# Kernel tuning notes

Measured on AMD Instinct MI355X. Metric: run time of the kernel, lower is better.

The kernel has to match this reference:

```python
import jax, jax.numpy as jnp
import numpy as np

B, G, S, L, F = 2, 1024, 64, 16, 8   # batch, attention windows, tokens/window, cells/token, in_features
ATT, RANK, HC = 128, 32, 32          # att_dim, factorization rank, n_head_channels
LF = L * F


def setup_inputs() -> dict:
    key = jax.random.key(0)
    ks = jax.random.split(key, 14)
    s = 0.05
    return {
        "x": jax.random.normal(ks[0], (B, G, S, L, F), jnp.float32),
        # rank-factorized Q projection: (L*F) -> att_dim
        "Wq_u": jax.random.normal(ks[1], (LF, RANK), jnp.float32) * s,
        "Wq_v": jax.random.normal(ks[2], (RANK, ATT), jnp.float32) * s,
        # rank-factorized KV projection: (L*F) -> 2*att_dim (bias=True in source)
        "Wkv_u": jax.random.normal(ks[3], (LF, RANK), jnp.float32) * s,
        "Wkv_v": jax.random.normal(ks[4], (RANK, 2 * ATT), jnp.float32) * s,
        "kv_b": jnp.zeros((2 * ATT,), jnp.float32),
        # rank-factorized out layer: att_dim -> (L*F)
        "Wo_u": jax.random.normal(ks[5], (ATT, RANK), jnp.float32) * s,
        "Wo_v": jax.random.normal(ks[6], (RANK, LF), jnp.float32) * s,
        # per-token-element residual gate (init 1e-7 as in source)
        "gamma": jnp.full((L, F), 1e-7, jnp.float32),
        # factorized MLP: (L*F) -> att_dim -> (L*F)
        "W1": jax.random.normal(ks[7], (LF, ATT), jnp.float32) * s,
        "b1": jnp.zeros((ATT,), jnp.float32),
        "W2": jax.random.normal(ks[8], (ATT, LF), jnp.float32) * s,
        "b2": jnp.zeros((LF,), jnp.float32),
        "gamma_mlp": jnp.full((), 1e-7, jnp.float32),
    }


def _ln(t):
    # layer norm over the token dims (L, F), no affine
    m = t.mean(axis=(-2, -1), keepdims=True)
    v = t.var(axis=(-2, -1), keepdims=True)
    return (t - m) * jax.lax.rsqrt(v + 1e-5)


def reference(x, Wq_u, Wq_v, Wkv_u, Wkv_v, kv_b, Wo_u, Wo_v, gamma, W1, b1, W2, b2, gamma_mlp):
    b, g, sfx, l, f = x.shape
    lf = l * f
    h = _ln(x).reshape(b, g, sfx, lf)                 # [b,g,s,LF]
    q = (h @ Wq_u) @ Wq_v                              # [b,g,s,ATT]
    kv = (h @ Wkv_u) @ Wkv_v + kv_b                    # [b,g,s,2*ATT]
    k, v = jnp.split(kv, 2, axis=-1)
    nh = q.shape[-1] // HC
    def heads(t):
        return t.reshape(b, g, sfx, nh, HC).transpose(0, 1, 3, 2, 4)  # [b,g,H,s,hc]
    qh, kh, vh = heads(q), heads(k), heads(v)
    scores = jnp.einsum('bghsc,bghtc->bghst', qh, kh) / np.float32(np.sqrt(HC))
    attn = jax.nn.softmax(scores, axis=-1)             # [b,g,H,s,s]
    o = jnp.einsum('bghst,bghtc->bghsc', attn, vh)
    o = o.transpose(0, 1, 3, 2, 4).reshape(b, g, sfx, nh * HC)
    upd = ((o @ Wo_u) @ Wo_v).reshape(b, g, sfx, l, f)
    x1 = x + gamma * upd                               # 'shift' update with gamma gate
    h2 = _ln(x1).reshape(b, g, sfx, lf)
    m = jax.nn.gelu(h2 @ W1 + b1) @ W2 + b2
    return x1 + gamma_mlp * m.reshape(b, g, sfx, l, f)
```

## Files before the change

### kernel.cpp

```cpp
#include <hip/hip_runtime.h>

#define NWIN 2048

#define WUT8_OFF 0
#define MT8_OFF  8192
#define OT8_OFF  12288
#define W1T_OFF  28672
#define W2T8_OFF 61440
#define CVEC_OFF 77824

typedef __attribute__((ext_vector_type(8))) __bf16 bf16x8;
typedef __attribute__((ext_vector_type(8))) short s16x8;
typedef __attribute__((ext_vector_type(4))) short s16x4;
typedef __attribute__((ext_vector_type(4))) float f32x4;

static __device__ inline short f2bf(float f) {
    __bf16 b = (__bf16)f;
    return __builtin_bit_cast(short, b);
}
static __device__ inline float bf2f(short h) {
    unsigned u = ((unsigned)(unsigned short)h) << 16;
    return __builtin_bit_cast(float, u);
}
static __device__ inline bf16x8 ldbf8(const short* p) {
    return __builtin_bit_cast(bf16x8, *(const s16x8*)p);
}
static __device__ inline unsigned char f2fp8(float v) {
    return (unsigned char)__builtin_amdgcn_cvt_pk_fp8_f32(v, v, 0u, false);
}
static __device__ inline long ld8(const void* p) {
    return *(const long*)p;
}

__global__ __launch_bounds__(256) void fam_pre(
    const float* __restrict__ Wq_u, const float* __restrict__ Wq_v,
    const float* __restrict__ Wkv_u, const float* __restrict__ Wkv_v,
    const float* __restrict__ kv_b, const float* __restrict__ Wo_u,
    const float* __restrict__ Wo_v, const float* __restrict__ W1,
    const float* __restrict__ W2, unsigned char* __restrict__ ws8)
{
    const int b = blockIdx.x, tid = threadIdx.x;
    float* cvec = (float*)(ws8 + CVEC_OFF);
    if (b < 16) {
        __shared__ float Wv[4096];
        __shared__ float Wu[4096];
        __shared__ float N[4096];
        for (int i = tid; i < 4096; i += 256) {
            int r = i >> 7, c = i & 127;
            Wv[i] = Wkv_v[r*256 + 128 + c];
            Wu[i] = Wo_u[i];
        }
        __syncthreads();
        for (int i = tid; i < 4096; i += 256) {
            int h = i >> 10, u = (i >> 5) & 31, r = i & 31;
            float acc = 0.f;
            for (int c = 0; c < 32; ++c) acc += Wv[r*128 + h*32 + c] * Wu[(h*32 + c)*32 + u];
            N[i] = acc;
        }
        __syncthreads();
        for (int i = tid; i < 1024; i += 256) {
            int jj = i >> 7, hr = i & 127;
            int j = b*8 + jj, h = hr >> 5, r = hr & 31;
            float acc = 0.f;
            for (int u = 0; u < 32; ++u) acc += N[h*1024 + u*32 + r] * Wo_v[u*128 + j];
            ws8[OT8_OFF + j*128 + hr] = f2fp8(acc * 128.f);
        }
    } else if (b < 32) {
        short* w1t = (short*)(ws8 + W1T_OFF);
        int i0 = (b - 16) * 8;
        for (int t = tid; t < 1024; t += 256) {
            int ii = t >> 7, k = t & 127, i = i0 + ii;
            w1t[i*128 + k] = f2bf(W1[k*128 + i]);
        }
    } else if (b < 48) {
        int j0 = (b - 32) * 8;
        for (int t = tid; t < 1024; t += 256) {
            int jj = t >> 7, k = t & 127, j = j0 + jj;
            ws8[W2T8_OFF + j*128 + k] = f2fp8(W2[k*128 + j] * 16.f);
        }
    } else {
        __shared__ float Aq[4096];
        __shared__ float Ak[4096];
        __shared__ float ov[32];
        for (int i = tid; i < 4096; i += 256) {
            int r = i >> 7, c = i & 127;
            Aq[i] = Wq_v[i];
            Ak[i] = Wkv_v[r*256 + c];
        }
        for (int i = tid; i < 8192; i += 256) {
            int n = i >> 7, k = i & 127;
            float w = (n < 32) ? Wq_u[k*32 + n] : Wkv_u[k*32 + (n - 32)];
            ws8[WUT8_OFF + n*128 + k] = f2fp8(w * 16.f);
        }
        __syncthreads();
        const float sc = 0.17677669529663687f * 256.f;
        for (int i = tid; i < 4096; i += 256) {
            int h = i >> 10, r = (i >> 5) & 31, u = i & 31;
            float acc = 0.f;
            for (int c = 0; c < 32; ++c) acc += Aq[u*128 + h*32 + c] * Ak[r*128 + h*32 + c];
            ws8[MT8_OFF + h*1024 + r*32 + u] = f2fp8(acc * sc);
        }
        if (tid < 32) {
            float a = 0.f;
            for (int att = 0; att < 128; ++att) a += kv_b[128 + att] * Wo_u[att*32 + tid];
            ov[tid] = a;
        }
        __syncthreads();
        if (tid < 128) {
            float a = 0.f;
            for (int u = 0; u < 32; ++u) a += ov[u] * Wo_v[u*128 + tid];
            cvec[tid] = a;
        }
    }
}

#define SRA 136
#define SHQ 40
#define SHB 72

#define SM_RA8   0
#define SM_HUQ8  8704
#define SM_KV8   11264
#define SM_KVT8  13824
#define SM_HB8   16128
#define SM_TOTAL 34560

__global__ __launch_bounds__(256, 4) void fam_main(
    const float* __restrict__ x, const unsigned char* __restrict__ ws8,
    const float* __restrict__ gamma, const float* __restrict__ b1,
    const float* __restrict__ b2, const float* __restrict__ gmlp_p,
    float* __restrict__ out)
{
    __shared__ __align__(16) unsigned char SM[SM_TOTAL];
    unsigned char* RA8  = SM + SM_RA8;
    unsigned char* HUQ8 = SM + SM_HUQ8;
    unsigned char* KV8  = SM + SM_KV8;
    unsigned char* KVT8 = SM + SM_KVT8;

    const float* cvec = (const float*)(ws8 + CVEC_OFF);
    const int tid = threadIdx.x;
    const int l   = tid & 63;
    const int wv  = tid >> 6;
    const int l15 = l & 15;
    const int lg  = l >> 4;
    const size_t base = (size_t)blockIdx.x * 8192;
    const float* __restrict__ xw   = x + base;
    float* __restrict__       outw = out + base;
    const int n0 = wv * 32;

    {
        int s = tid >> 2, c = tid & 3;
        float4 xr1[8];
        float sum = 0.f, sq = 0.f;
        #pragma unroll
        for (int j = 0; j < 8; ++j) {
            xr1[j] = *(const float4*)&xw[s*128 + c*32 + j*4];
            sum += xr1[j].x + xr1[j].y + xr1[j].z + xr1[j].w;
            sq  += xr1[j].x*xr1[j].x + xr1[j].y*xr1[j].y + xr1[j].z*xr1[j].z + xr1[j].w*xr1[j].w;
        }
        sum += __shfl_xor(sum, 1); sq += __shfl_xor(sq, 1);
        sum += __shfl_xor(sum, 2); sq += __shfl_xor(sq, 2);
        float mean = sum * (1.f/128.f);
        float var  = sq * (1.f/128.f) - mean*mean;
        float rinv = rsqrtf(var + 1e-5f);
        #pragma unroll
        for (int j = 0; j < 8; ++j) {
            unsigned w = 0;
            w = __builtin_amdgcn_cvt_pk_fp8_f32((xr1[j].x - mean)*rinv, (xr1[j].y - mean)*rinv, w, false);
            w = __builtin_amdgcn_cvt_pk_fp8_f32((xr1[j].z - mean)*rinv, (xr1[j].w - mean)*rinv, w, true);
            *(unsigned*)&RA8[s*SRA + c*32 + j*4] = w;
        }
    }
    __syncthreads();

    {
        long bfr[4];
        #pragma unroll
        for (int kb = 0; kb < 4; ++kb)
            bfr[kb] = ld8(ws8 + WUT8_OFF + (wv*16 + l15)*128 + kb*32 + lg*8);
        #pragma unroll
        for (int m = 0; m < 4; ++m) {
            f32x4 acc = {0.f, 0.f, 0.f, 0.f};
            #pragma unroll
            for (int kb = 0; kb < 4; ++kb) {
                long a = ld8(RA8 + (m*16 + l15)*SRA + kb*32 + lg*8);
                acc = __builtin_amdgcn_mfma_f32_16x16x32_fp8_fp8(a, bfr[kb], acc, 0, 0, 0);
            }
            if (wv < 2) {
                int col = wv*16 + l15;
                #pragma unroll
                for (int j = 0; j < 4; ++j)
                    HUQ8[(m*16 + lg*4 + j)*SHQ + col] = f2fp8(acc[j] * 0.25f);
            } else {
                int u = (wv - 2)*16 + l15;
                #pragma unroll
                for (int j = 0; j < 4; ++j)
                    KV8[(m*16 + lg*4 + j)*SHQ + u] = f2fp8(acc[j] * 0.25f);
                unsigned w = 0;
                w = __builtin_amdgcn_cvt_pk_fp8_f32(acc[0]*0.25f, acc[1]*0.25f, w, false);
                w = __builtin_amdgcn_cvt_pk_fp8_f32(acc[2]*0.25f, acc[3]*0.25f, w, true);
                *(unsigned*)&KVT8[u*SHB + m*16 + lg*4] = w;
            }
        }
    }
    __syncthreads();

    {
        const int h = wv;
        unsigned char* HB8h = SM + SM_HB8 + h*4608;
        long bm0 = ld8(ws8 + MT8_OFF + h*1024 + l15*32 + lg*8);
        long bm1 = ld8(ws8 + MT8_OFF + h*1024 + (16 + l15)*32 + lg*8);
        #pragma unroll
        for (int m = 0; m < 4; ++m) {
            long aq = ld8(HUQ8 + (m*16 + l15)*SHQ + lg*8);
            f32x4 z = {0.f, 0.f, 0.f, 0.f};
            f32x4 a0 = __builtin_amdgcn_mfma_f32_16x16x32_fp8_fp8(aq, bm0, z, 0, 0, 0);
            f32x4 a1 = __builtin_amdgcn_mfma_f32_16x16x32_fp8_fp8(aq, bm1, z, 0, 0, 0);
            #pragma unroll
            for (int j = 0; j < 4; ++j) {
                int row = (m*16 + lg*4 + j)*SHB;
                HB8h[row + l15]      = f2fp8(a0[j] * 0.0625f);
                HB8h[row + 16 + l15] = f2fp8(a1[j] * 0.0625f);
            }
        }
        long av[4], bq[4];
        #pragma unroll
        for (int m = 0; m < 4; ++m) av[m] = ld8(KV8 + (m*16 + l15)*SHQ + lg*8);
        #pragma unroll
        for (int n = 0; n < 4; ++n) bq[n] = ld8(HB8h + (n*16 + l15)*SHB + lg*8);
        f32x4 cc[4][4];
        #pragma unroll
        for (int m = 0; m < 4; ++m)
            #pragma unroll
            for (int n = 0; n < 4; ++n) {
                f32x4 z = {0.f, 0.f, 0.f, 0.f};
                cc[m][n] = __builtin_amdgcn_mfma_f32_16x16x32_fp8_fp8(av[m], bq[n], z, 0, 0, 0);
            }
        const float c1 = 0.0056355275f;
        #pragma unroll
        for (int n = 0; n < 4; ++n) {
            float e[4][4];
            float sm = 0.f;
            #pragma unroll
            for (int m = 0; m < 4; ++m)
                #pragma unroll
                for (int j = 0; j < 4; ++j) {
                    e[m][j] = exp2f(fminf(cc[m][n][j] * c1, 43.f));
                    sm += e[m][j];
                }
            sm += __shfl_xor(sm, 16);
            sm += __shfl_xor(sm, 32);
            float rs64 = __builtin_amdgcn_rcpf(sm) * 64.f;
            int srow = (n*16 + l15) * SHB;
            #pragma unroll
            for (int m = 0; m < 4; ++m) {
                unsigned w = 0;
                w = __builtin_amdgcn_cvt_pk_fp8_f32(e[m][0]*rs64, e[m][1]*rs64, w, false);
                w = __builtin_amdgcn_cvt_pk_fp8_f32(e[m][2]*rs64, e[m][3]*rs64, w, true);
                *(unsigned*)&HB8h[srow + m*16 + lg*4] = w;
            }
        }
        long a8[4][2], b8[2][2];
        #pragma unroll
        for (int m = 0; m < 4; ++m)
            #pragma unroll
            for (int kb = 0; kb < 2; ++kb)
                a8[m][kb] = ld8(HB8h + (m*16 + l15)*SHB + kb*32 + lg*8);
        #pragma unroll
        for (int nn = 0; nn < 2; ++nn)
            #pragma unroll
            for (int kb = 0; kb < 2; ++kb)
                b8[nn][kb] = ld8(KVT8 + (nn*16 + l15)*SHB + kb*32 + lg*8);
        #pragma unroll
        for (int m = 0; m < 4; ++m)
            #pragma unroll
            for (int nn = 0; nn < 2; ++nn) {
                f32x4 acc = {0.f,0.f,0.f,0.f};
                acc = __builtin_amdgcn_mfma_f32_16x16x32_fp8_fp8(a8[m][0], b8[nn][0], acc, 0, 0, 0);
                acc = __builtin_amdgcn_mfma_f32_16x16x32_fp8_fp8(a8[m][1], b8[nn][1], acc, 0, 0, 0);
                #pragma unroll
                for (int j = 0; j < 4; ++j)
                    RA8[(m*16 + lg*4 + j)*SRA + h*32 + nn*16 + l15] = f2fp8(acc[j] * 0.03125f);
            }
    }
    __syncthreads();

    float x1v[4][2][4];
    short* XB = (short*)(SM + SM_HB8);

    {
        float xr[4][2][4];
        #pragma unroll
        for (int m = 0; m < 4; ++m)
            #pragma unroll
            for (int nn = 0; nn < 2; ++nn)
                #pragma unroll
                for (int j = 0; j < 4; ++j)
                    xr[m][nn][j] = xw[(m*16 + lg*4 + j)*128 + n0 + nn*16 + l15];
        long bo[2][4];
        float cv[2], gm[2];
        #pragma unroll
        for (int nn = 0; nn < 2; ++nn) {
            int col = n0 + nn*16 + l15;
            #pragma unroll
            for (int kb = 0; kb < 4; ++kb)
                bo[nn][kb] = ld8(ws8 + OT8_OFF + col*128 + kb*32 + lg*8);
            cv[nn] = cvec[col];
            gm[nn] = gamma[col];
        }
        f32x4 acc[4][2];
        #pragma unroll
        for (int m = 0; m < 4; ++m)
            #pragma unroll
            for (int nn = 0; nn < 2; ++nn) acc[m][nn] = (f32x4){0.f,0.f,0.f,0.f};
        #pragma unroll
        for (int m = 0; m < 4; ++m) {
            long a[4];
            #pragma unroll
            for (int kb = 0; kb < 4; ++kb)
                a[kb] = ld8(RA8 + (m*16 + l15)*SRA + kb*32 + lg*8);
            #pragma unroll
            for (int kb = 0; kb < 4; ++kb)
                #pragma unroll
                for (int nn = 0; nn < 2; ++nn)
                    acc[m][nn] = __builtin_amdgcn_mfma_f32_16x16x32_fp8_fp8(a[kb], bo[nn][kb], acc[m][nn], 0, 0, 0);
        }
        #pragma unroll
        for (int m = 0; m < 4; ++m)
            #pragma unroll
            for (int nn = 0; nn < 2; ++nn)
                #pragma unroll
                for (int j = 0; j < 4; ++j) {
                    int row = m*16 + lg*4 + j;
                    float v = xr[m][nn][j] + gm[nn] * (acc[m][nn][j] * 9.765625e-4f + cv[nn]);
                    x1v[m][nn][j] = v;
                    XB[row*SRA + n0 + nn*16 + l15] = f2bf(v);
                }
    }
    __syncthreads();

    {
        int s = tid >> 2, c = tid & 3;
        float sum = 0.f, sq = 0.f;
        #pragma unroll
        for (int jj = 0; jj < 8; ++jj) {
            s16x4 hv = *(const s16x4*)&XB[s*SRA + c*32 + jj*4];
            #pragma unroll
            for (int e = 0; e < 4; ++e) {
                float f = bf2f(hv[e]);
                sum += f; sq += f*f;
            }
        }
        sum += __shfl_xor(sum, 1); sq += __shfl_xor(sq, 1);
        sum += __shfl_xor(sum, 2); sq += __shfl_xor(sq, 2);
        float mean = sum * (1.f/128.f);
        float var  = sq * (1.f/128.f) - mean*mean;
        float rinv = rsqrtf(var + 1e-5f);
        #pragma unroll
        for (int jj = 0; jj < 8; ++jj) {
            s16x4 hv = *(const s16x4*)&XB[s*SRA + c*32 + jj*4];
            s16x4 ov;
            #pragma unroll
            for (int e = 0; e < 4; ++e) ov[e] = f2bf((bf2f(hv[e]) - mean) * rinv);
            *(s16x4*)&XB[s*SRA + c*32 + jj*4] = ov;
        }
    }
    __syncthreads();

    {
        const short* W1t = (const short*)(ws8 + W1T_OFF);
        bf16x8 bw1[2][4];
        float bb1[2];
        #pragma unroll
        for (int nn = 0; nn < 2; ++nn) {
            #pragma unroll
            for (int k = 0; k < 4; ++k)
                bw1[nn][k] = ldbf8(&((const short*)(ws8 + W1T_OFF))[(n0 + nn*16 + l15)*128 + k*32 + lg*8]);
            bb1[nn] = b1[n0 + nn*16 + l15];
        }
        (void)W1t;
        #pragma unroll
        for (int m = 0; m < 4; ++m) {
            bf16x8 a[4];
            #pragma unroll
            for (int k = 0; k < 4; ++k)
                a[k] = ldbf8(&XB[(m*16 + l15)*SRA + k*32 + lg*8]);
            #pragma unroll
            for (int nn = 0; nn < 2; ++nn) {
                f32x4 acc = {0.f,0.f,0.f,0.f};
                #pragma unroll
                for (int k = 0; k < 4; ++k)
                    acc = __builtin_amdgcn_mfma_f32_16x16x32_bf16(a[k], bw1[nn][k], acc, 0, 0, 0);
                #pragma unroll
                for (int j = 0; j < 4; ++j) {
                    float t = acc[j] + bb1[nn];
                    float u2 = t*t;
                    float p = fmaf(-0.1029417f, u2, -2.3021622f);
                    float g = t * __builtin_amdgcn_rcpf(1.f + exp2f(t*p));
                    RA8[(m*16 + lg*4 + j)*SRA + n0 + nn*16 + l15] = f2fp8(g * 8.f);
                }
            }
        }
    }
    __syncthreads();

    {
        const float gmv = gmlp_p[0];
        long bw[2][4];
        float bb[2];
        #pragma unroll
        for (int nn = 0; nn < 2; ++nn) {
            int col = n0 + nn*16 + l15;
            #pragma unroll
            for (int kb = 0; kb < 4; ++kb)
                bw[nn][kb] = ld8(ws8 + W2T8_OFF + col*128 + kb*32 + lg*8);
            bb[nn] = b2[col];
        }
        #pragma unroll
        for (int m = 0; m < 4; ++m) {
            long a[4];
            #pragma unroll
            for (int kb = 0; kb < 4; ++kb)
                a[kb] = ld8(RA8 + (m*16 + l15)*SRA + kb*32 + lg*8);
            #pragma unroll
            for (int nn = 0; nn < 2; ++nn) {
                f32x4 acc = {0.f,0.f,0.f,0.f};
                #pragma unroll
                for (int kb = 0; kb < 4; ++kb)
                    acc = __builtin_amdgcn_mfma_f32_16x16x32_fp8_fp8(a[kb], bw[nn][kb], acc, 0, 0, 0);
                #pragma unroll
                for (int j = 0; j < 4; ++j)
                    outw[(m*16 + lg*4 + j)*128 + n0 + nn*16 + l15] =
                        x1v[m][nn][j] + gmv * (acc[j] * 0.0078125f + bb[nn]);
            }
        }
    }
}

extern "C" void kernel_launch(void* const* d_in, const int* in_sizes, int n_in,
                              void* d_out, int out_size, void* d_ws, size_t ws_size,
                              hipStream_t stream) {
    const float* x     = (const float*)d_in[0];
    const float* Wq_u  = (const float*)d_in[1];
    const float* Wq_v  = (const float*)d_in[2];
    const float* Wkv_u = (const float*)d_in[3];
    const float* Wkv_v = (const float*)d_in[4];
    const float* kv_b  = (const float*)d_in[5];
    const float* Wo_u  = (const float*)d_in[6];
    const float* Wo_v  = (const float*)d_in[7];
    const float* gamma = (const float*)d_in[8];
    const float* W1    = (const float*)d_in[9];
    const float* b1    = (const float*)d_in[10];
    const float* W2    = (const float*)d_in[11];
    const float* b2    = (const float*)d_in[12];
    const float* gmlp  = (const float*)d_in[13];
    unsigned char* ws8 = (unsigned char*)d_ws;
    float* out = (float*)d_out;

    fam_pre<<<49, 256, 0, stream>>>(Wq_u, Wq_v, Wkv_u, Wkv_v, kv_b, Wo_u, Wo_v, W1, W2, ws8);
    fam_main<<<NWIN, 256, 0, stream>>>(x, ws8, gamma, b1, b2, gmlp, out);
}
```

Before: 94.16 us.

## Defer softmax normalization via ones-row MFMA computing row sums

Replaces the per-row softmax sum reduction (shuffles plus reciprocal before the fp8 quantization) with unnormalized exponentials, using a fixed offset and clamp to keep them in fp8 range. Row sums are obtained by an extra MFMA against a ones-filled block (0x48 is 1.0 in fp8 e4m3) appended to the transposed V buffer. The output is then normalized after the PV product. This removes cross-lane shuffles and the serial dependence of the score stage on the sum, at the cost of more shared memory, extra MFMAs, and precision risk from unnormalized fp8 probabilities.

```diff
diff --git a/kernel.cpp b/kernel.cpp
--- a/kernel.cpp
+++ b/kernel.cpp
@@ -122,8 +122,8 @@
 #define SM_HUQ8  8704
 #define SM_KV8   11264
 #define SM_KVT8  13824
-#define SM_HB8   16128
-#define SM_TOTAL 34560
+#define SM_HB8   17280
+#define SM_TOTAL 35712
 
 __global__ __launch_bounds__(256, 4) void fam_main(
     const float* __restrict__ x, const unsigned char* __restrict__ ws8,
@@ -148,6 +148,10 @@
     float* __restrict__       outw = out + base;
     const int n0 = wv * 32;
 
+    if (tid < 72) {
+        unsigned* p = (unsigned*)(KVT8 + 32*SHB + tid*16);
+        p[0] = 0x48484848u; p[1] = 0x48484848u; p[2] = 0x48484848u; p[3] = 0x48484848u;
+    }
     {
         int s = tid >> 2, c = tid & 3;
         float4 xr1[8];
@@ -239,28 +243,20 @@
         const float c1 = 0.0056355275f;
         #pragma unroll
         for (int n = 0; n < 4; ++n) {
-            float e[4][4];
-            float sm = 0.f;
-            #pragma unroll
-            for (int m = 0; m < 4; ++m)
-                #pragma unroll
-                for (int j = 0; j < 4; ++j) {
-                    e[m][j] = exp2f(fminf(cc[m][n][j] * c1, 43.f));
-                    sm += e[m][j];
-                }
-            sm += __shfl_xor(sm, 16);
-            sm += __shfl_xor(sm, 32);
-            float rs64 = __builtin_amdgcn_rcpf(sm) * 64.f;
             int srow = (n*16 + l15) * SHB;
             #pragma unroll
             for (int m = 0; m < 4; ++m) {
+                float e0 = exp2f(fminf(fmaf(cc[m][n][0], c1, 6.f), 14.f));
+                float e1 = exp2f(fminf(fmaf(cc[m][n][1], c1, 6.f), 14.f));
+                float e2 = exp2f(fminf(fmaf(cc[m][n][2], c1, 6.f), 14.f));
+                float e3 = exp2f(fminf(fmaf(cc[m][n][3], c1, 6.f), 14.f));
                 unsigned w = 0;
-                w = __builtin_amdgcn_cvt_pk_fp8_f32(e[m][0]*rs64, e[m][1]*rs64, w, false);
-                w = __builtin_amdgcn_cvt_pk_fp8_f32(e[m][2]*rs64, e[m][3]*rs64, w, true);
+                w = __builtin_amdgcn_cvt_pk_fp8_f32(e0, e1, w, false);
+                w = __builtin_amdgcn_cvt_pk_fp8_f32(e2, e3, w, true);
                 *(unsigned*)&HB8h[srow + m*16 + lg*4] = w;
             }
         }
-        long a8[4][2], b8[2][2];
+        long a8[4][2], b8[2][2], bs[2];
         #pragma unroll
         for (int m = 0; m < 4; ++m)
             #pragma unroll
@@ -272,16 +268,28 @@
             for (int kb = 0; kb < 2; ++kb)
                 b8[nn][kb] = ld8(KVT8 + (nn*16 + l15)*SHB + kb*32 + lg*8);
         #pragma unroll
-        for (int m = 0; m < 4; ++m)
+        for (int kb = 0; kb < 2; ++kb)
+            bs[kb] = ld8(KVT8 + (32 + l15)*SHB + kb*32 + lg*8);
+        #pragma unroll
+        for (int m = 0; m < 4; ++m) {
+            f32x4 accs = {0.f,0.f,0.f,0.f};
+            accs = __builtin_amdgcn_mfma_f32_16x16x32_fp8_fp8(a8[m][0], bs[0], accs, 0, 0, 0);
+            accs = __builtin_amdgcn_mfma_f32_16x16x32_fp8_fp8(a8[m][1], bs[1], accs, 0, 0, 0);
+            f32x4 acc[2];
             #pragma unroll
             for (int nn = 0; nn < 2; ++nn) {
-                f32x4 acc = {0.f,0.f,0.f,0.f};
-                acc = __builtin_amdgcn_mfma_f32_16x16x32_fp8_fp8(a8[m][0], b8[nn][0], acc, 0, 0, 0);
-                acc = __builtin_amdgcn_mfma_f32_16x16x32_fp8_fp8(a8[m][1], b8[nn][1], acc, 0, 0, 0);
-                #pragma unroll
-                for (int j = 0; j < 4; ++j)
-                    RA8[(m*16 + lg*4 + j)*SRA + h*32 + nn*16 + l15] = f2fp8(acc[j] * 0.03125f);
-            }
+                acc[nn] = (f32x4){0.f,0.f,0.f,0.f};
+                acc[nn] = __builtin_amdgcn_mfma_f32_16x16x32_fp8_fp8(a8[m][0], b8[nn][0], acc[nn], 0, 0, 0);
+                acc[nn] = __builtin_amdgcn_mfma_f32_16x16x32_fp8_fp8(a8[m][1], b8[nn][1], acc[nn], 0, 0, 0);
+            }
+            #pragma unroll
+            for (int j = 0; j < 4; ++j) {
+                float rs8 = 8.f * __builtin_amdgcn_rcpf(accs[j]);
+                int row = (m*16 + lg*4 + j)*SRA + h*32;
+                RA8[row + l15]      = f2fp8(acc[0][j] * rs8);
+                RA8[row + 16 + l15] = f2fp8(acc[1][j] * rs8);
+            }
+        }
     }
     __syncthreads();
 
@@ -368,7 +376,6 @@
     __syncthreads();
 
     {
-        const short* W1t = (const short*)(ws8 + W1T_OFF);
         bf16x8 bw1[2][4];
         float bb1[2];
         #pragma unroll
@@ -378,7 +385,6 @@
                 bw1[nn][k] = ldbf8(&((const short*)(ws8 + W1T_OFF))[(n0 + nn*16 + l15)*128 + k*32 + lg*8]);
             bb1[nn] = b1[n0 + nn*16 + l15];
         }
-        (void)W1t;
         #pragma unroll
         for (int m = 0; m < 4; ++m) {
             bf16x8 a[4];
```

Result: no change. 93.36 us (-0.8%).
